# Performance work log

Measured on AMD Instinct MI355X. Metric: run time of the kernel, lower is better.

The kernel has to match this reference:

```python
import jax, jax.numpy as jnp
import numpy as np

M = 8
EPS = 1e-5


def _bn(x, gamma, beta):
    # x: [T, N, C]; torch BatchNorm1d on [T, C, N] (training mode) normalizes
    # over batch and length dims -> axes (0, 1) here, biased variance.
    mean = jnp.mean(x, axis=(0, 1))
    var = jnp.var(x, axis=(0, 1))
    return (x - mean) * jax.lax.rsqrt(var + EPS) * gamma + beta


def setup_inputs() -> dict:
    key = jax.random.key(0)
    T, N, E = 128, 256, 128
    ks = jax.random.split(key, 16)
    s = 1.0 / np.sqrt(E)
    inp = {
        "node": jax.random.normal(ks[0], (T, N, E), dtype=jnp.float32),
        "Wq": jax.random.uniform(ks[1], (E, E), jnp.float32, -s, s),
        "bq": jax.random.uniform(ks[2], (E,), jnp.float32, -s, s),
        "Wk": jax.random.uniform(ks[3], (E, E), jnp.float32, -s, s),
        "bk": jax.random.uniform(ks[4], (E,), jnp.float32, -s, s),
        "Wv": jax.random.uniform(ks[5], (E, E), jnp.float32, -s, s),
        "bv": jax.random.uniform(ks[6], (E,), jnp.float32, -s, s),
        "Ww": jax.random.uniform(ks[7], (E, E), jnp.float32, -s, s),
        "bw": jax.random.uniform(ks[8], (E,), jnp.float32, -s, s),
        "Wf1": jax.random.uniform(ks[9], (4 * E, E), jnp.float32, -s, s),
        "bf1": jax.random.uniform(ks[10], (4 * E,), jnp.float32, -s, s),
        "Wf2": jax.random.uniform(ks[11], (E, 4 * E), jnp.float32, -0.5 * s, 0.5 * s),
        "bf2": jax.random.uniform(ks[12], (E,), jnp.float32, -0.5 * s, 0.5 * s),
        "g1": jnp.ones((E,), jnp.float32),
        "be1": jnp.zeros((E,), jnp.float32),
        "g2": jnp.ones((E,), jnp.float32),
        "be2": jnp.zeros((E,), jnp.float32),
        "temp_len": T,
    }
    return inp


def reference(node, Wq, bq, Wk, bk, Wv, bv, Ww, bw, Wf1, bf1, Wf2, bf2,
              g1, be1, g2, be2, temp_len):
    T, N, E = node.shape
    D = E // M          # head dim = 16
    dk = E / M          # softmax scale denominator (embedding_size / M)

    q = (node @ Wq.T + bq).reshape(T, N, M, D)
    k = (node @ Wk.T + bk).reshape(T, N, M, D)
    v = (node @ Wv.T + bv).reshape(T, N, M, D)

    # scores[t,n,j,m] = sum_d q[t,n,m,d]*k[t,j,m,d] / sqrt(dk)
    scores = jnp.einsum('tnmd,tjmd->tnjm', q, k) / jnp.sqrt(jnp.float32(dk))
    attn = jax.nn.softmax(scores, axis=2)  # softmax over key dim (dim=2)

    # out[t,n,m,d] = sum_j attn[t,n,j,m] * v[t,j,m,d]
    out = jnp.einsum('tnjm,tjmd->tnmd', attn, v).reshape(T, N, E)

    x = out @ Ww.T + bw + node
    x = _bn(x, g1, be1)

    x1 = jax.nn.relu(x @ Wf1.T + bf1) @ Wf2.T + bf2
    x = x + x1
    x = _bn(x, g2, be2)
    return x
```

## Files before the change

### kernel.cpp

```cpp
#include <hip/hip_runtime.h>
#include <stdint.h>

typedef unsigned int  uint32;
typedef unsigned short u16;
typedef __attribute__((ext_vector_type(8))) short short8;
typedef __attribute__((ext_vector_type(4))) float f32x4;
typedef __attribute__((ext_vector_type(4))) _Float16 half4;

__device__ __forceinline__ float bits2f(uint32 u){ union{uint32 u; float f;} c; c.u=u; return c.f; }
__device__ __forceinline__ uint32 f2bits(float f){ union{uint32 u; float f;} c; c.f=f; return c.u; }
__device__ __forceinline__ u16 f2b(float f){ uint32 u=f2bits(f); return (u16)((u + 0x7FFFu + ((u>>16)&1u))>>16); }
__device__ __forceinline__ float b2f(u16 h){ return bits2f(((uint32)h)<<16); }
__device__ __forceinline__ u16 f2h(float f){ _Float16 h=(_Float16)f; union{u16 u; _Float16 h;} c; c.h=h; return c.u; }
__device__ __forceinline__ float4 ld4f(const float* p){ return *(const float4*)p; }
#define BLO(u) bits2f((u)<<16)
#define BHI(u) bits2f((u)&0xFFFF0000u)

#define QKS 24

__device__ __forceinline__ void load_ab(const float* __restrict__ gacc,
                                        const float* __restrict__ gam,
                                        const float* __restrict__ bet,
                                        float* sA, float* sB, int t)
{
  if (t < 128) {
    const float mean = gacc[t] * (1.f/32768.f);
    const float var  = gacc[128 + t] * (1.f/32768.f) - mean * mean;
    const float rstd = rsqrtf(var + 1e-5f);
    const float Ac = gam[t] * rstd;
    sA[t] = Ac;
    sB[t] = bet[t] - mean * Ac;
  }
  __syncthreads();
}

template<int OMODE, int RES, bool RELU, bool AF32, bool WF32, bool BNA, bool STATS, int JT>
__device__ __forceinline__ void gemm_tile(
    u16* As, u16* Ws, const float* sA, const float* sB, float* pS, float* pQ,
    const void* Ain, const void* W, const float* bias, const void* res,
    float* gacc_out, void* out, int row0, int col0, int K, int Nout,
    float oscale, int t)
{
  constexpr int WROWS = JT * 32;
  const int L = t & 63, w = t >> 6;
  const int wrow = (w >> 1) * 64, wcol = (w & 1) * (JT * 16);
  const int lm = L & 15, lg = L >> 4;

  f32x4 acc[4][JT];
#pragma unroll
  for (int i = 0; i < 4; ++i)
#pragma unroll
    for (int j = 0; j < JT; ++j) acc[i][j] = (f32x4){0.f,0.f,0.f,0.f};

  const int srow = t >> 1, skc = (t & 1) * 32;
  const u16*   Ab = (const u16*)Ain + (size_t)(row0 + srow) * K + skc;
  const float* Af = (const float*)Ain + (size_t)(row0 + srow) * K + skc;
  u16* Asp = As + srow * 72 + skc;
  constexpr int TPR = 256 / WROWS;
  const int wsrow = t / TPR, wskc = (t % TPR) * (64 / TPR);
  const u16*   Wp  = (const u16*)W + (size_t)(col0 + wsrow) * K + wskc;
  const float* Wpf = (const float*)W + (size_t)(col0 + wsrow) * K + wskc;
  u16* Wsp = Ws + wsrow * 72 + wskc;
  constexpr int NW = (64 / TPR) / 8;

  short8 ga[4]; short8 gw[NW];
  float4 fa[4][2]; float4 fw[NW][2];

  auto load_chunk = [&](int k0) {
    if constexpr (AF32) {
#pragma unroll
      for (int i = 0; i < 4; ++i) {
        fa[i][0] = ld4f(Af + k0 + i*8);
        fa[i][1] = ld4f(Af + k0 + i*8 + 4);
      }
    } else {
#pragma unroll
      for (int i = 0; i < 4; ++i) ga[i] = *(const short8*)(Ab + k0 + i*8);
    }
    if constexpr (WF32) {
#pragma unroll
      for (int i = 0; i < NW; ++i) {
        fw[i][0] = ld4f(Wpf + k0 + i*8);
        fw[i][1] = ld4f(Wpf + k0 + i*8 + 4);
      }
    } else {
#pragma unroll
      for (int i = 0; i < NW; ++i) gw[i] = *(const short8*)(Wp + k0 + i*8);
    }
  };

  auto write_chunk = [&](int k0) {
    if constexpr (AF32) {
#pragma unroll
      for (int i = 0; i < 4; ++i) {
        short8 s;
        s[0]=(short)f2b(fa[i][0].x); s[1]=(short)f2b(fa[i][0].y);
        s[2]=(short)f2b(fa[i][0].z); s[3]=(short)f2b(fa[i][0].w);
        s[4]=(short)f2b(fa[i][1].x); s[5]=(short)f2b(fa[i][1].y);
        s[6]=(short)f2b(fa[i][1].z); s[7]=(short)f2b(fa[i][1].w);
        *(short8*)(Asp + i*8) = s;
      }
    } else if constexpr (BNA) {
#pragma unroll
      for (int i = 0; i < 4; ++i) {
        const int c = skc + k0 + i*8;
        const short8 x8 = ga[i];
        const float4 A0 = *(const float4*)&sA[c], A1 = *(const float4*)&sA[c+4];
        const float4 B0 = *(const float4*)&sB[c], B1 = *(const float4*)&sB[c+4];
        short8 s;
        s[0]=(short)f2b(b2f((u16)x8[0])*A0.x+B0.x); s[1]=(short)f2b(b2f((u16)x8[1])*A0.y+B0.y);
        s[2]=(short)f2b(b2f((u16)x8[2])*A0.z+B0.z); s[3]=(short)f2b(b2f((u16)x8[3])*A0.w+B0.w);
        s[4]=(short)f2b(b2f((u16)x8[4])*A1.x+B1.x); s[5]=(short)f2b(b2f((u16)x8[5])*A1.y+B1.y);
        s[6]=(short)f2b(b2f((u16)x8[6])*A1.z+B1.z); s[7]=(short)f2b(b2f((u16)x8[7])*A1.w+B1.w);
        *(short8*)(Asp + i*8) = s;
      }
    } else {
#pragma unroll
      for (int i = 0; i < 4; ++i) *(short8*)(Asp + i*8) = ga[i];
    }
    if constexpr (WF32) {
#pragma unroll
      for (int i = 0; i < NW; ++i) {
        short8 s;
        s[0]=(short)f2b(fw[i][0].x); s[1]=(short)f2b(fw[i][0].y);
        s[2]=(short)f2b(fw[i][0].z); s[3]=(short)f2b(fw[i][0].w);
        s[4]=(short)f2b(fw[i][1].x); s[5]=(short)f2b(fw[i][1].y);
        s[6]=(short)f2b(fw[i][1].z); s[7]=(short)f2b(fw[i][1].w);
        *(short8*)(Wsp + i*8) = s;
      }
    } else {
#pragma unroll
      for (int i = 0; i < NW; ++i) *(short8*)(Wsp + i*8) = gw[i];
    }
  };

  load_chunk(0);
  for (int k0 = 0; k0 < K; k0 += 64) {
    __syncthreads();
    write_chunk(k0);
    __syncthreads();
    if (k0 + 64 < K) load_chunk(k0 + 64);
#pragma unroll
    for (int ks = 0; ks < 64; ks += 32) {
      short8 af[4], wf[JT];
#pragma unroll
      for (int i = 0; i < 4; ++i)
        af[i] = *(const short8*)(As + (wrow + i*16 + lm) * 72 + ks + lg*8);
#pragma unroll
      for (int j = 0; j < JT; ++j)
        wf[j] = *(const short8*)(Ws + (wcol + j*16 + lm) * 72 + ks + lg*8);
#pragma unroll
      for (int i = 0; i < 4; ++i)
#pragma unroll
        for (int j = 0; j < JT; ++j)
          acc[i][j] = __builtin_amdgcn_mfma_f32_16x16x32_bf16(af[i], wf[j], acc[i][j], 0, 0, 0);
    }
  }

  float bj[JT];
#pragma unroll
  for (int j = 0; j < JT; ++j) bj[j] = bias[col0 + wcol + j*16 + lm];

  float stS[JT], stQ[JT];
#pragma unroll
  for (int j = 0; j < JT; ++j) { stS[j] = 0.f; stQ[j] = 0.f; }

#pragma unroll
  for (int i = 0; i < 4; ++i) {
    const int rowb = row0 + wrow + i*16 + lg*4;
#pragma unroll
    for (int j = 0; j < JT; ++j) {
      const int col = col0 + wcol + j*16 + lm;
      float ra = 0.f, rb = 0.f;
      if constexpr (RES == 3) { ra = sA[col & 127]; rb = sB[col & 127]; }
      if constexpr (OMODE == 3) {
        const int tt = rowb >> 8, n0 = rowb & 255;
        const int mh = col >> 4, d = col & 15;
        uint2 o;
        o.x = (uint32)f2h(acc[i][j][0] + bj[j]) | ((uint32)f2h(acc[i][j][1] + bj[j]) << 16);
        o.y = (uint32)f2h(acc[i][j][2] + bj[j]) | ((uint32)f2h(acc[i][j][3] + bj[j]) << 16);
        *(uint2*)((u16*)out + (((size_t)tt*8 + mh)*16 + d)*256 + n0) = o;
      } else {
#pragma unroll
        for (int r = 0; r < 4; ++r) {
          const int row = rowb + r;
          float v = acc[i][j][r] + bj[j];
          if constexpr (RES == 1) v += ((const float*)res)[(size_t)row*128 + col];
          if constexpr (RES == 3) v += b2f(((const u16*)res)[(size_t)row*128 + col]) * ra + rb;
          if constexpr (RELU) v = fmaxf(v, 0.f);
          if constexpr (STATS) { stS[j] += v; stQ[j] += v*v; }
          if constexpr (OMODE == 2) {
            const int tt = row >> 8, n = row & 255, mh = col >> 4, d = col & 15;
            ((u16*)out)[(((size_t)tt*8 + mh)*256 + n)*16 + d] = f2h(v * oscale);
          } else {
            ((u16*)out)[(size_t)row * Nout + col] = f2b(v);
          }
        }
      }
    }
  }

  if constexpr (STATS) {
    __syncthreads();
    if (t < 128) { pS[t] = 0.f; pQ[t] = 0.f; }
    __syncthreads();
#pragma unroll
    for (int j = 0; j < JT; ++j) {
      const int col = col0 + wcol + j*16 + lm;
      atomicAdd(&pS[col], stS[j]);
      atomicAdd(&pQ[col], stQ[j]);
    }
    __syncthreads();
    if (t < 128) {
      atomicAdd(&gacc_out[t],       pS[t]);
      atomicAdd(&gacc_out[128 + t], pQ[t]);
    }
  }
}

__global__ __launch_bounds__(256)
void qkv_k(const float* __restrict__ node,
           const float* __restrict__ Wq, const float* __restrict__ bq,
           const float* __restrict__ Wk, const float* __restrict__ bk,
           const float* __restrict__ Wv, const float* __restrict__ bv,
           const float* __restrict__ Ww, const float* __restrict__ Wf1,
           const float* __restrict__ Wf2,
           u16* __restrict__ qb, u16* __restrict__ kb, u16* __restrict__ vb,
           u16* __restrict__ wb, float* __restrict__ accbuf)
{
  const int bid = blockIdx.x, t = threadIdx.x;
  if (bid < 768) {
    __shared__ u16 As[128*72];
    __shared__ u16 Ws[128*72];
    __shared__ __align__(16) float sA[128], sB[128];
    __shared__ float pS[128], pQ[128];
    const int x = bid & 255, y = bid >> 8;
    const float QSCALE = 0.36067376022224085f;
    if (y == 0)
      gemm_tile<2,0,false,true,true,false,false,4>(As,Ws,sA,sB,pS,pQ, node, Wq, bq,
          nullptr, nullptr, qb, x*128, 0, 128, 128, QSCALE, t);
    else if (y == 1)
      gemm_tile<2,0,false,true,true,false,false,4>(As,Ws,sA,sB,pS,pQ, node, Wk, bk,
          nullptr, nullptr, kb, x*128, 0, 128, 128, 1.f, t);
    else
      gemm_tile<3,0,false,true,true,false,false,4>(As,Ws,sA,sB,pS,pQ, node, Wv, bv,
          nullptr, nullptr, vb, x*128, 0, 128, 128, 1.f, t);
  } else if (bid < 912) {
    const int i = (bid - 768) * 256 + t;
    const float4* src; u16* dst;
    if      (i <  4096) { src = (const float4*)Ww  + i;         dst = wb +  49152 + (size_t)i*4; }
    else if (i < 20480) { src = (const float4*)Wf1 + (i-4096);  dst = wb +  65536 + (size_t)(i-4096)*4; }
    else                { src = (const float4*)Wf2 + (i-20480); dst = wb + 131072 + (size_t)(i-20480)*4; }
    float4 v = *src;
    uint2 o;
    o.x = (uint32)f2b(v.x) | ((uint32)f2b(v.y) << 16);
    o.y = (uint32)f2b(v.z) | ((uint32)f2b(v.w) << 16);
    *(uint2*)dst = o;
  } else {
    accbuf[t] = 0.f;
    accbuf[256 + t] = 0.f;
  }
}

__global__ __launch_bounds__(256)
void oproj_k(const u16* __restrict__ ab, const u16* __restrict__ wwb,
             const float* __restrict__ bw, const float* __restrict__ node,
             float* __restrict__ accbuf, u16* __restrict__ xb)
{
  __shared__ u16 As[128*72];
  __shared__ u16 Ws[64*72];
  __shared__ __align__(16) float sA[128], sB[128];
  __shared__ float pS[128], pQ[128];
  gemm_tile<0,1,false,false,false,false,true,2>(As,Ws,sA,sB,pS,pQ, ab, wwb, bw,
      node, accbuf, xb, blockIdx.x*128, blockIdx.y*64, 128, 128, 1.f, threadIdx.x);
}

#define HS2_LD 264
#define AS_LD 136
#define WS_LD 72

__global__ __launch_bounds__(512, 4)
void ffn_k(const u16* __restrict__ xb, const u16* __restrict__ wf1b,
           const float* __restrict__ bf1, const u16* __restrict__ wf2b,
           const float* __restrict__ bf2, const float* __restrict__ accbuf,
           const float* __restrict__ g1, const float* __restrict__ be1,
           float* __restrict__ acc2, u16* __restrict__ x2b)
{
  __shared__ u16 Hs[64*HS2_LD];
  __shared__ u16 As[64*AS_LD];
  __shared__ u16 Ws[128*WS_LD];
  __shared__ __align__(16) float sA[128], sB[128];
  __shared__ float pS[128], pQ[128];

  const int t = threadIdx.x;
  const int row0 = blockIdx.x * 64;
  load_ab(accbuf, g1, be1, sA, sB, t);

  {
    const int r = t >> 3, seg = (t & 7) * 16;
    const u16* src = xb + (size_t)(row0 + r) * 128 + seg;
    u16* dst = As + r * AS_LD + seg;
#pragma unroll
    for (int h = 0; h < 2; ++h) {
      const short8 x8 = *(const short8*)(src + h*8);
      const int c = seg + h*8;
      const float4 A0 = *(const float4*)&sA[c], A1 = *(const float4*)&sA[c+4];
      const float4 B0 = *(const float4*)&sB[c], B1 = *(const float4*)&sB[c+4];
      short8 s;
      s[0]=(short)f2b(b2f((u16)x8[0])*A0.x+B0.x); s[1]=(short)f2b(b2f((u16)x8[1])*A0.y+B0.y);
      s[2]=(short)f2b(b2f((u16)x8[2])*A0.z+B0.z); s[3]=(short)f2b(b2f((u16)x8[3])*A0.w+B0.w);
      s[4]=(short)f2b(b2f((u16)x8[4])*A1.x+B1.x); s[5]=(short)f2b(b2f((u16)x8[5])*A1.y+B1.y);
      s[6]=(short)f2b(b2f((u16)x8[6])*A1.z+B1.z); s[7]=(short)f2b(b2f((u16)x8[7])*A1.w+B1.w);
      *(short8*)(dst + h*8) = s;
    }
  }

  const int w = t >> 6, L = t & 63, lm = L & 15, lg = L >> 4;
  const int wcol = w * 16;
  const int wr = t >> 2, kc = (t & 3) * 16;

  auto wsrc = [&](int g) -> const u16* {
    const int half = g >> 3, cc = g & 7;
    if (cc < 4) return wf1b + (size_t)((2*half + (cc>>1))*128 + wr)*128 + (cc&1)*64 + kc;
    return wf2b + (size_t)wr*512 + half*256 + (cc-4)*64 + kc;
  };

  f32x4 accF[4];
  f32x4 acc2r[4];
#pragma unroll
  for (int i = 0; i < 4; ++i) {
    accF[i]  = (f32x4){0.f,0.f,0.f,0.f};
    acc2r[i] = (f32x4){0.f,0.f,0.f,0.f};
  }

  short8 gw0 = *(const short8*)(wsrc(0));
  short8 gw1 = *(const short8*)(wsrc(0) + 8);

  for (int g = 0; g < 16; ++g) {
    const int cc = g & 7;
    const bool is1 = (cc < 4);
    __syncthreads();
    *(short8*)(Ws + wr*WS_LD + kc)     = gw0;
    *(short8*)(Ws + wr*WS_LD + kc + 8) = gw1;
    __syncthreads();
    if (g < 15) {
      gw0 = *(const short8*)(wsrc(g+1));
      gw1 = *(const short8*)(wsrc(g+1) + 8);
    }
    const u16* Abase = is1 ? (As + ((size_t)(cc & 1) * 64))
                           : (Hs + ((size_t)(cc - 4) * 64));
    const int ald = is1 ? AS_LD : HS2_LD;
#pragma unroll
    for (int ks = 0; ks < 64; ks += 32) {
      short8 af[4], wf;
#pragma unroll
      for (int i = 0; i < 4; ++i)
        af[i] = *(const short8*)(Abase + (i*16 + lm) * ald + ks + lg*8);
      wf = *(const short8*)(Ws + (wcol + lm) * WS_LD + ks + lg*8);
      if (is1) {
#pragma unroll
        for (int i = 0; i < 4; ++i)
          accF[i] = __builtin_amdgcn_mfma_f32_16x16x32_bf16(af[i], wf, accF[i], 0, 0, 0);
      } else {
#pragma unroll
        for (int i = 0; i < 4; ++i)
          acc2r[i] = __builtin_amdgcn_mfma_f32_16x16x32_bf16(af[i], wf, acc2r[i], 0, 0, 0);
      }
    }
    if (is1 && (cc & 1)) {
      const int half = g >> 3;
      const int ct = 2*half + (cc >> 1);
      const int lct = cc >> 1;
      const float b1 = bf1[ct*128 + wcol + lm];
#pragma unroll
      for (int i = 0; i < 4; ++i) {
#pragma unroll
        for (int r = 0; r < 4; ++r) {
          const int row = i*16 + lg*4 + r;
          Hs[row*HS2_LD + lct*128 + wcol + lm] = f2b(fmaxf(accF[i][r] + b1, 0.f));
        }
        accF[i] = (f32x4){0.f,0.f,0.f,0.f};
      }
    }
  }

  const int col = wcol + lm;
  const float b2 = bf2[col];
  const float ra = sA[col], rb = sB[col];
  float stS = 0.f, stQ = 0.f;
#pragma unroll
  for (int i = 0; i < 4; ++i) {
#pragma unroll
    for (int r = 0; r < 4; ++r) {
      const int row = row0 + i*16 + lg*4 + r;
      float v = acc2r[i][r] + b2 + b2f(xb[(size_t)row*128 + col]) * ra + rb;
      stS += v; stQ += v*v;
      x2b[(size_t)row*128 + col] = f2b(v);
    }
  }
  __syncthreads();
  if (t < 128) { pS[t] = 0.f; pQ[t] = 0.f; }
  __syncthreads();
  atomicAdd(&pS[col], stS);
  atomicAdd(&pQ[col], stQ);
  __syncthreads();
  if (t < 128) {
    atomicAdd(&acc2[t],       pS[t]);
    atomicAdd(&acc2[128 + t], pQ[t]);
  }
}

__global__ __launch_bounds__(256)
void attn_k(const u16* __restrict__ q, const u16* __restrict__ k,
            const u16* __restrict__ v, u16* __restrict__ ab)
{
  __shared__ __align__(16) u16 Qs[256*QKS];
  __shared__ __align__(16) u16 Ks[256*QKS];
  __shared__ __align__(16) u16 Vt[16*264];
  const int tm = blockIdx.x, tt = tm >> 3, m = tm & 7;
  const int t = threadIdx.x;

  const uint4* qg = (const uint4*)(q + (size_t)tm*4096);
  const uint4* kg = (const uint4*)(k + (size_t)tm*4096);
  const uint4* vg = (const uint4*)(v + (size_t)tm*4096);
#pragma unroll
  for (int p = t; p < 512; p += 256) {
    const uint4 a = qg[p], b = kg[p], c = vg[p];
    const int row = p >> 1, h = (p & 1) * 8;
    *(uint4*)(Qs + row*QKS + h) = a;
    *(uint4*)(Ks + row*QKS + h) = b;
    *(uint4*)(Vt + (p >> 5)*264 + (p & 31)*8) = c;
  }
  __syncthreads();

  const int w = t >> 6, L = t & 63, lm = L & 15, quad = L >> 4;

  half4 vf[16];
#pragma unroll
  for (int jt = 0; jt < 16; ++jt)
    vf[jt] = *(const half4*)(Vt + lm*264 + jt*16 + quad*4);

  for (int nt = 0; nt < 4; ++nt) {
    const half4 bq = *(const half4*)(Qs + ((w*4 + nt)*16 + lm)*QKS + quad*4);
    f32x4 s[16];
#pragma unroll
    for (int jt = 0; jt < 16; ++jt) {
      const half4 af = *(const half4*)(Ks + (jt*16 + lm)*QKS + quad*4);
      s[jt] = __builtin_amdgcn_mfma_f32_16x16x16f16(af, bq, (f32x4){0.f,0.f,0.f,0.f}, 0, 0, 0);
    }
    float mx = s[0][0];
#pragma unroll
    for (int jt = 0; jt < 16; ++jt)
#pragma unroll
      for (int r = 0; r < 4; ++r) mx = fmaxf(mx, s[jt][r]);
    mx = fmaxf(mx, __shfl_xor(mx, 16));
    mx = fmaxf(mx, __shfl_xor(mx, 32));
    float ls = 0.f;
#pragma unroll
    for (int jt = 0; jt < 16; ++jt)
#pragma unroll
      for (int r = 0; r < 4; ++r) { const float p = exp2f(s[jt][r] - mx); s[jt][r] = p; ls += p; }
    ls += __shfl_xor(ls, 16);
    ls += __shfl_xor(ls, 32);

    f32x4 oacc = {0.f,0.f,0.f,0.f};
#pragma unroll
    for (int jt = 0; jt < 16; ++jt) {
      half4 pf;
      pf[0] = (_Float16)s[jt][0]; pf[1] = (_Float16)s[jt][1];
      pf[2] = (_Float16)s[jt][2]; pf[3] = (_Float16)s[jt][3];
      oacc = __builtin_amdgcn_mfma_f32_16x16x16f16(pf, vf[jt], oacc, 0, 0, 0);
    }
    const int q0 = w*64 + nt*16 + quad*4;
#pragma unroll
    for (int r = 0; r < 4; ++r) {
      const float lr = __shfl(ls, quad*4 + r);
      ab[((size_t)tt*256 + q0 + r)*128 + m*16 + lm] = f2b(oacc[r] / lr);
    }
  }
}

__global__ __launch_bounds__(256)
void bn_final(const uint2* __restrict__ x2, const float* __restrict__ gacc,
              const float* __restrict__ gam, const float* __restrict__ bet,
              float* __restrict__ out)
{
  __shared__ __align__(16) float sA[128], sB[128];
  const int t = threadIdx.x;
  load_ab(gacc, gam, bet, sA, sB, t);
#pragma unroll 2
  for (int kk = 0; kk < 8; ++kk) {
    const size_t idx = (size_t)blockIdx.x * 2048 + kk * 256 + t;
    const uint2 u = x2[idx];
    const int c = (int)((idx & 31) * 4);
    const f32x4 A = *(const f32x4*)&sA[c];
    const f32x4 B = *(const f32x4*)&sB[c];
    f32x4 o;
    o[0] = BLO(u.x)*A[0] + B[0];
    o[1] = BHI(u.x)*A[1] + B[1];
    o[2] = BLO(u.y)*A[2] + B[2];
    o[3] = BHI(u.y)*A[3] + B[3];
    *(f32x4*)(out + idx*4) = o;
  }
}

extern "C" void kernel_launch(void* const* d_in, const int* in_sizes, int n_in,
                              void* d_out, int out_size, void* d_ws, size_t ws_size,
                              hipStream_t stream)
{
  (void)in_sizes; (void)n_in; (void)out_size; (void)ws_size;
  const float* node = (const float*)d_in[0];
  const float* Wq  = (const float*)d_in[1];  const float* bq  = (const float*)d_in[2];
  const float* Wk  = (const float*)d_in[3];  const float* bk  = (const float*)d_in[4];
  const float* Wv  = (const float*)d_in[5];  const float* bv  = (const float*)d_in[6];
  const float* Ww  = (const float*)d_in[7];  const float* bw  = (const float*)d_in[8];
  const float* Wf1 = (const float*)d_in[9];  const float* bf1 = (const float*)d_in[10];
  const float* Wf2 = (const float*)d_in[11]; const float* bf2 = (const float*)d_in[12];
  const float* g1  = (const float*)d_in[13]; const float* be1 = (const float*)d_in[14];
  const float* g2  = (const float*)d_in[15]; const float* be2 = (const float*)d_in[16];
  float* out = (float*)d_out;
  char* ws = (char*)d_ws;

  u16* wb  = (u16*)(ws + 0);
  u16* qb  = (u16*)(ws + 524288);
  u16* kb  = (u16*)(ws + 8912896);
  u16* vb  = (u16*)(ws + 17301504);
  u16* ab  = (u16*)(ws + 25690112);
  u16* xb  = (u16*)(ws + 34078720);
  u16* x2b = (u16*)(ws + 42467328);
  float* accbuf = (float*)(ws + 50855936);

  u16* wwb = wb + 49152;  u16* wf1b = wb + 65536; u16* wf2b = wb + 131072;

  dim3 blk(256);

  qkv_k<<<dim3(913), blk, 0, stream>>>(node, Wq,bq, Wk,bk, Wv,bv, Ww, Wf1, Wf2,
                                       qb, kb, vb, wb, accbuf);
  attn_k<<<dim3(1024), blk, 0, stream>>>(qb, kb, vb, ab);
  oproj_k<<<dim3(256,2), blk, 0, stream>>>(ab, wwb, bw, node, accbuf, xb);
  ffn_k<<<dim3(512), dim3(512), 0, stream>>>(xb, wf1b, bf1, wf2b, bf2,
                                             accbuf, g1, be1, accbuf + 256, x2b);
  bn_final<<<dim3(512), blk, 0, stream>>>((const uint2*)x2b, accbuf + 256, g2, be2, out);
}
```

Measured before the change: 200.4 us.

## Fuse Q/K/V projections into one block per row tile reusing staged node

```diff
diff --git a/kernel.cpp b/kernel.cpp
--- a/kernel.cpp
+++ b/kernel.cpp
@@ -229,24 +229,130 @@
            u16* __restrict__ wb, float* __restrict__ accbuf)
 {
   const int bid = blockIdx.x, t = threadIdx.x;
-  if (bid < 768) {
-    __shared__ u16 As[128*72];
-    __shared__ u16 Ws[128*72];
-    __shared__ __align__(16) float sA[128], sB[128];
-    __shared__ float pS[128], pQ[128];
-    const int x = bid & 255, y = bid >> 8;
-    const float QSCALE = 0.36067376022224085f;
-    if (y == 0)
-      gemm_tile<2,0,false,true,true,false,false,4>(As,Ws,sA,sB,pS,pQ, node, Wq, bq,
-          nullptr, nullptr, qb, x*128, 0, 128, 128, QSCALE, t);
-    else if (y == 1)
-      gemm_tile<2,0,false,true,true,false,false,4>(As,Ws,sA,sB,pS,pQ, node, Wk, bk,
-          nullptr, nullptr, kb, x*128, 0, 128, 128, 1.f, t);
-    else
-      gemm_tile<3,0,false,true,true,false,false,4>(As,Ws,sA,sB,pS,pQ, node, Wv, bv,
-          nullptr, nullptr, vb, x*128, 0, 128, 128, 1.f, t);
-  } else if (bid < 912) {
-    const int i = (bid - 768) * 256 + t;
+  if (bid < 256) {
+    __shared__ u16 As[2*128*72];
+    __shared__ u16 Ws[2*128*72];
+    const int row0 = bid * 128;
+    const int L = t & 63, w = t >> 6;
+    const int wrow = (w >> 1) * 64, wcol = (w & 1) * 64;
+    const int lm = L & 15, lg = L >> 4;
+    const int srow = t >> 1, skc = (t & 1) * 32;
+
+    {
+      const float* Af = node + (size_t)(row0 + srow) * 128 + skc;
+#pragma unroll
+      for (int c = 0; c < 2; ++c) {
+        u16* Asp = As + c*128*72 + srow*72 + skc;
+#pragma unroll
+        for (int i = 0; i < 4; ++i) {
+          const float4 fa = ld4f(Af + c*64 + i*8);
+          const float4 fb = ld4f(Af + c*64 + i*8 + 4);
+          short8 s;
+          s[0]=(short)f2b(fa.x); s[1]=(short)f2b(fa.y); s[2]=(short)f2b(fa.z); s[3]=(short)f2b(fa.w);
+          s[4]=(short)f2b(fb.x); s[5]=(short)f2b(fb.y); s[6]=(short)f2b(fb.z); s[7]=(short)f2b(fb.w);
+          *(short8*)(Asp + i*8) = s;
+        }
+      }
+    }
+
+    const float* WY0 = Wq; const float* WY1 = Wk; const float* WY2 = Wv;
+    float4 fw[4][2];
+    {
+      const float* Wp = WY0 + (size_t)srow*128 + skc;
+#pragma unroll
+      for (int i = 0; i < 4; ++i) { fw[i][0] = ld4f(Wp + i*8); fw[i][1] = ld4f(Wp + i*8 + 4); }
+    }
+
+    f32x4 acc[4][4];
+#pragma unroll
+    for (int i = 0; i < 4; ++i)
+#pragma unroll
+      for (int j = 0; j < 4; ++j) acc[i][j] = (f32x4){0.f,0.f,0.f,0.f};
+
+    for (int g = 0; g < 6; ++g) {
+      u16* Wsp = Ws + (g&1)*128*72 + srow*72 + skc;
+#pragma unroll
+      for (int i = 0; i < 4; ++i) {
+        short8 s;
+        s[0]=(short)f2b(fw[i][0].x); s[1]=(short)f2b(fw[i][0].y);
+        s[2]=(short)f2b(fw[i][0].z); s[3]=(short)f2b(fw[i][0].w);
+        s[4]=(short)f2b(fw[i][1].x); s[5]=(short)f2b(fw[i][1].y);
+        s[6]=(short)f2b(fw[i][1].z); s[7]=(short)f2b(fw[i][1].w);
+        *(short8*)(Wsp + i*8) = s;
+      }
+      __syncthreads();
+      if (g < 5) {
+        const int gn = g + 1;
+        const float* WYn = (gn < 2) ? WY0 : (gn < 4) ? WY1 : WY2;
+        const float* Wp = WYn + (size_t)srow*128 + (gn & 1)*64 + skc;
+#pragma unroll
+        for (int i = 0; i < 4; ++i) { fw[i][0] = ld4f(Wp + i*8); fw[i][1] = ld4f(Wp + i*8 + 4); }
+      }
+      const u16* Ab = As + (g&1)*128*72;
+      const u16* Wb = Ws + (g&1)*128*72;
+#pragma unroll
+      for (int ks = 0; ks < 64; ks += 32) {
+        short8 af[4], wf[4];
+#pragma unroll
+        for (int i = 0; i < 4; ++i)
+          af[i] = *(const short8*)(Ab + (wrow + i*16 + lm) * 72 + ks + lg*8);
+#pragma unroll
+        for (int j = 0; j < 4; ++j)
+          wf[j] = *(const short8*)(Wb + (wcol + j*16 + lm) * 72 + ks + lg*8);
+#pragma unroll
+        for (int i = 0; i < 4; ++i)
+#pragma unroll
+          for (int j = 0; j < 4; ++j)
+            acc[i][j] = __builtin_amdgcn_mfma_f32_16x16x32_bf16(af[i], wf[j], acc[i][j], 0, 0, 0);
+      }
+      if (g & 1) {
+        const int y = g >> 1;
+        const float* bias = (y == 0) ? bq : (y == 1) ? bk : bv;
+        u16* outp = (y == 0) ? qb : (y == 1) ? kb : vb;
+        const float osc = (y == 0) ? 0.36067376022224085f : 1.f;
+        float bj[4];
+#pragma unroll
+        for (int j = 0; j < 4; ++j) bj[j] = bias[wcol + j*16 + lm];
+        if (y < 2) {
+#pragma unroll
+          for (int i = 0; i < 4; ++i) {
+            const int rowb = row0 + wrow + i*16 + lg*4;
+#pragma unroll
+            for (int j = 0; j < 4; ++j) {
+              const int col = wcol + j*16 + lm;
+              const int mh = col >> 4, d = col & 15;
+#pragma unroll
+              for (int r = 0; r < 4; ++r) {
+                const int row = rowb + r;
+                const int tt2 = row >> 8, n = row & 255;
+                outp[(((size_t)tt2*8 + mh)*256 + n)*16 + d] = f2h((acc[i][j][r] + bj[j]) * osc);
+              }
+            }
+          }
+        } else {
+#pragma unroll
+          for (int i = 0; i < 4; ++i) {
+            const int rowb = row0 + wrow + i*16 + lg*4;
+            const int tt2 = rowb >> 8, n0 = rowb & 255;
+#pragma unroll
+            for (int j = 0; j < 4; ++j) {
+              const int col = wcol + j*16 + lm;
+              const int mh = col >> 4, d = col & 15;
+              uint2 o;
+              o.x = (uint32)f2h(acc[i][j][0] + bj[j]) | ((uint32)f2h(acc[i][j][1] + bj[j]) << 16);
+              o.y = (uint32)f2h(acc[i][j][2] + bj[j]) | ((uint32)f2h(acc[i][j][3] + bj[j]) << 16);
+              *(uint2*)(outp + (((size_t)tt2*8 + mh)*16 + d)*256 + n0) = o;
+            }
+          }
+        }
+#pragma unroll
+        for (int i = 0; i < 4; ++i)
+#pragma unroll
+          for (int j = 0; j < 4; ++j) acc[i][j] = (f32x4){0.f,0.f,0.f,0.f};
+      }
+    }
+  } else if (bid < 400) {
+    const int i = (bid - 256) * 256 + t;
     const float4* src; u16* dst;
     if      (i <  4096) { src = (const float4*)Ww  + i;         dst = wb +  49152 + (size_t)i*4; }
     else if (i < 20480) { src = (const float4*)Wf1 + (i-4096);  dst = wb +  65536 + (size_t)(i-4096)*4; }
@@ -534,7 +640,7 @@
 
   dim3 blk(256);
 
-  qkv_k<<<dim3(913), blk, 0, stream>>>(node, Wq,bq, Wk,bk, Wv,bv, Ww, Wf1, Wf2,
+  qkv_k<<<dim3(401), blk, 0, stream>>>(node, Wq,bq, Wk,bk, Wv,bv, Ww, Wf1, Wf2,
                                        qb, kb, vb, wb, accbuf);
   attn_k<<<dim3(1024), blk, 0, stream>>>(qb, kb, vb, ab);
   oproj_k<<<dim3(256,2), blk, 0, stream>>>(ab, wwb, bw, node, accbuf, xb);
```

Measured after the change: 200.4 us (median of 2 runs). About the same (+0.0%).
